# Performance work log

Measured on AMD Instinct MI355X. Metric: run time of the kernel, lower is better.

## Reference

```python
import jax, jax.numpy as jnp
import numpy as np

D_MODEL = 1024
NHEAD = 16
DIM_HEAD = 64
SCALE = DIM_HEAD ** (-0.5)


def setup_inputs() -> dict:
    key = jax.random.key(0)
    ks = jax.random.split(key, 8)
    B, N = 2, 2048
    inner = NHEAD * DIM_HEAD
    s = 0.02
    return {
        "query": jax.random.normal(ks[0], (B, N, D_MODEL), jnp.float32),
        "key": jax.random.normal(ks[1], (B, N, D_MODEL), jnp.float32),
        "value": jax.random.normal(ks[2], (B, N, D_MODEL), jnp.float32),
        "Wq": jax.random.normal(ks[3], (D_MODEL, inner), jnp.float32) * s,
        "Wk": jax.random.normal(ks[4], (D_MODEL, inner), jnp.float32) * s,
        "Wv": jax.random.normal(ks[5], (D_MODEL, inner), jnp.float32) * s,
        "Wo": jax.random.normal(ks[6], (inner, D_MODEL), jnp.float32) * s,
        "bo": jnp.zeros((D_MODEL,), jnp.float32),
    }


def reference(query, key, value, Wq, Wk, Wv, Wo, bo):
    B, Nq, _ = query.shape
    Nk = key.shape[1]
    # projections (no bias), split heads: [B, N, h, d]
    q = (query @ Wq).reshape(B, Nq, NHEAD, DIM_HEAD)
    k = (key @ Wk).reshape(B, Nk, NHEAD, DIM_HEAD)
    v = (value @ Wv).reshape(B, Nk, NHEAD, DIM_HEAD)
    # scores [B, h, Nq, Nk]
    sim = jnp.einsum('bihd,bjhd->bhij', q, k) * SCALE
    attn = jax.nn.softmax(sim, axis=-1)  # dropout p=0.0 -> identity
    out = jnp.einsum('bhij,bjhd->bihd', attn, v).reshape(B, Nq, NHEAD * DIM_HEAD)
    return out @ Wo + bo
```

## Files before the change

kernel.cpp:

```cpp
#include <hip/hip_runtime.h>
#include <stdint.h>

typedef __attribute__((ext_vector_type(8))) short short8;
typedef __attribute__((ext_vector_type(8))) unsigned short ushort8;
typedef __attribute__((ext_vector_type(4))) unsigned short ushort4v;
typedef __attribute__((ext_vector_type(4))) float float4v;
typedef _Float16 half4v __attribute__((ext_vector_type(4)));

#define D_MODEL 1024
#define NHEAD 16
#define DIM_HEAD 64
#define BATCH 2
#define SEQ 2048
#define BH (BATCH*NHEAD)
#define MROWS (BATCH*SEQ)
#define MK ((size_t)MROWS * D_MODEL)

__device__ __forceinline__ unsigned short f2bf(float f) {
  union { float f; unsigned u; } v; v.f = f;
  unsigned r = v.u + 0x7fffu + ((v.u >> 16) & 1u);
  return (unsigned short)(r >> 16);
}
__device__ __forceinline__ unsigned short f2bf_fast(float f) {
  union { float f; unsigned u; } v; v.f = f;
  return (unsigned short)((v.u + 0x8000u) >> 16);
}
__device__ __forceinline__ unsigned pk2bf(float a, float b) {
  union { float f; unsigned u; } x, y; x.f = a; y.f = b;
  return __builtin_amdgcn_perm(y.u + 0x8000u, x.u + 0x8000u, 0x07060302u);
}

__device__ __forceinline__ void gld16(const unsigned short* g, unsigned short* l) {
  __builtin_amdgcn_global_load_lds(
      (const __attribute__((address_space(1))) unsigned int*)g,
      (__attribute__((address_space(3))) unsigned int*)l, 16, 0, 0);
}

__global__ __launch_bounds__(256) void wtrans_kernel(const float* __restrict__ Wq,
    const float* __restrict__ Wk, const float* __restrict__ Wv,
    const float* __restrict__ Wo, unsigned short* __restrict__ WT0) {
  __shared__ float tile[32][33];
  const int z = blockIdx.z;
  const float* W = (z == 0) ? Wq : (z == 1) ? Wk : (z == 2) ? Wv : Wo;
  const float scale = (z == 0) ? 0.125f : 1.0f;
  unsigned short* WT = WT0 + ((size_t)z << 20);
  int bn = blockIdx.x * 32;
  int bk = blockIdx.y * 32;
  int tx = threadIdx.x & 31, ty = threadIdx.x >> 5;
#pragma unroll
  for (int i = 0; i < 4; i++)
    tile[ty + i*8][tx] = W[(size_t)(bk + ty + i*8) * D_MODEL + bn + tx];
  __syncthreads();
#pragma unroll
  for (int i = 0; i < 4; i++)
    WT[(size_t)(bn + ty + i*8) * D_MODEL + bk + tx] = f2bf(tile[tx][ty + i*8] * scale);
}

__global__ __launch_bounds__(256) void cast_kernel(const float* __restrict__ q,
    const float* __restrict__ k, const float* __restrict__ v,
    unsigned short* __restrict__ out) {
  const float* src = (blockIdx.y == 0) ? q : (blockIdx.y == 1) ? k : v;
  unsigned short* dst = out + (size_t)blockIdx.y * MK;
  size_t idx = ((size_t)blockIdx.x * 256 + threadIdx.x) * 8;
  float4v a = *(const float4v*)(src + idx);
  float4v b = *(const float4v*)(src + idx + 4);
  ushort8 o;
  o[0] = f2bf(a[0]); o[1] = f2bf(a[1]); o[2] = f2bf(a[2]); o[3] = f2bf(a[3]);
  o[4] = f2bf(b[0]); o[5] = f2bf(b[1]); o[6] = f2bf(b[2]); o[7] = f2bf(b[3]);
  *(ushort8*)(dst + idx) = o;
}

__global__ __launch_bounds__(256) void vtrans_kernel(const unsigned short* __restrict__ Vh,
                                                     unsigned short* __restrict__ VT) {
  __shared__ unsigned short tile[64][72];
  const int bh = blockIdx.x;
  const int n0 = blockIdx.y * 64;
  const int t = threadIdx.x;
#pragma unroll
  for (int p = 0; p < 2; p++) {
    int g = p*256 + t; int row = g >> 3, c = g & 7;
    *(ushort8*)&tile[row][c*8] =
      *(const ushort8*)(Vh + ((size_t)(bh*SEQ + n0 + row))*DIM_HEAD + c*8);
  }
  __syncthreads();
  int d = t >> 2, kc = (t & 3) * 16;
  ushort8 o0, o1;
#pragma unroll
  for (int j = 0; j < 8; j++) { o0[j] = tile[kc + j][d]; o1[j] = tile[kc + 8 + j][d]; }
  unsigned short* dst = VT + (((size_t)(bh*(SEQ/64) + blockIdx.y))*DIM_HEAD + d)*64 + kc;
  *(ushort8*)dst = o0;
  *(ushort8*)(dst + 8) = o1;
}

__global__ __launch_bounds__(256, 3) void proj_kernel(const unsigned short* __restrict__ Xbf,
    const unsigned short* __restrict__ WT0, unsigned short* __restrict__ Y0) {
  __shared__ unsigned short Al[128*64];
  __shared__ unsigned short Bl[128*64];
  const int z = blockIdx.z;
  const unsigned short* A  = Xbf + (size_t)z * MK;
  const unsigned short* BT = WT0 + ((size_t)z << 20);
  unsigned short* Y = Y0 + (size_t)z * MK;
  const int m0 = blockIdx.x * 128, n0 = blockIdx.y * 128;
  const int t = threadIdx.x;
  const int lane = t & 63, w = t >> 6, quad = lane >> 4, lid = lane & 15;
  const int wm = w & 1, wn = w >> 1;
  const int r8 = lane >> 3, c8 = (lane & 7) * 8;

  float4v acc[4][4];
#pragma unroll
  for (int i = 0; i < 4; i++)
#pragma unroll
    for (int j = 0; j < 4; j++) acc[i][j] = (float4v)0.0f;

  for (int k0 = 0; k0 < D_MODEL; k0 += 64) {
#pragma unroll
    for (int p = 0; p < 4; p++) {
      int seg = w*4 + p;
      gld16(A  + (size_t)(m0 + seg*8 + r8) * D_MODEL + k0 + c8, &Al[seg*8*64]);
      gld16(BT + (size_t)(n0 + seg*8 + r8) * D_MODEL + k0 + c8, &Bl[seg*8*64]);
    }
    __syncthreads();
#pragma unroll
    for (int kst = 0; kst < 2; kst++) {
      short8 af[4], bfr[4];
#pragma unroll
      for (int i = 0; i < 4; i++)
        af[i] = *(const short8*)&Al[(wm*64 + i*16 + lid)*64 + kst*32 + quad*8];
#pragma unroll
      for (int j = 0; j < 4; j++)
        bfr[j] = *(const short8*)&Bl[(wn*64 + j*16 + lid)*64 + kst*32 + quad*8];
#pragma unroll
      for (int i = 0; i < 4; i++)
#pragma unroll
        for (int j = 0; j < 4; j++)
          acc[i][j] = __builtin_amdgcn_mfma_f32_16x16x32_bf16(af[i], bfr[j], acc[i][j], 0, 0, 0);
    }
    __syncthreads();
  }
#pragma unroll
  for (int i = 0; i < 4; i++)
#pragma unroll
    for (int j = 0; j < 4; j++)
#pragma unroll
      for (int r = 0; r < 4; r++) {
        int row = m0 + wm*64 + i*16 + quad*4 + r;
        int col = n0 + wn*64 + j*16 + lid;
        int b = row >> 11, n = row & (SEQ - 1);
        int h = col >> 6,  d = col & 63;
        Y[(((size_t)(b*NHEAD + h))*SEQ + n)*DIM_HEAD + d] = f2bf_fast(acc[i][j][r]);
      }
}

__global__ __launch_bounds__(256, 3) void outproj_kernel(const unsigned short* __restrict__ A,
    const unsigned short* __restrict__ WT, const float* __restrict__ bias,
    float* __restrict__ out) {
  __shared__ unsigned short Al[64*64];
  __shared__ unsigned short Bl[128*64];
  const int m0 = blockIdx.x * 64, n0 = blockIdx.y * 128;
  const int t = threadIdx.x;
  const int lane = t & 63, w = t >> 6, quad = lane >> 4, lid = lane & 15;
  const int wm = w & 1, wn = w >> 1;
  const int r8 = lane >> 3, c8 = (lane & 7) * 8;

  float4v acc[2][4];
#pragma unroll
  for (int i = 0; i < 2; i++)
#pragma unroll
    for (int j = 0; j < 4; j++) acc[i][j] = (float4v)0.0f;

  for (int k0 = 0; k0 < D_MODEL; k0 += 64) {
#pragma unroll
    for (int p = 0; p < 2; p++) {
      int seg = w*2 + p;
      gld16(A + (size_t)(m0 + seg*8 + r8) * D_MODEL + k0 + c8, &Al[seg*8*64]);
    }
#pragma unroll
    for (int p = 0; p < 4; p++) {
      int seg = w*4 + p;
      gld16(WT + (size_t)(n0 + seg*8 + r8) * D_MODEL + k0 + c8, &Bl[seg*8*64]);
    }
    __syncthreads();
#pragma unroll
    for (int kst = 0; kst < 2; kst++) {
      short8 af[2], bfr[4];
#pragma unroll
      for (int i = 0; i < 2; i++)
        af[i] = *(const short8*)&Al[(wm*32 + i*16 + lid)*64 + kst*32 + quad*8];
#pragma unroll
      for (int j = 0; j < 4; j++)
        bfr[j] = *(const short8*)&Bl[(wn*64 + j*16 + lid)*64 + kst*32 + quad*8];
#pragma unroll
      for (int i = 0; i < 2; i++)
#pragma unroll
        for (int j = 0; j < 4; j++)
          acc[i][j] = __builtin_amdgcn_mfma_f32_16x16x32_bf16(af[i], bfr[j], acc[i][j], 0, 0, 0);
    }
    __syncthreads();
  }
#pragma unroll
  for (int i = 0; i < 2; i++)
#pragma unroll
    for (int j = 0; j < 4; j++)
#pragma unroll
      for (int r = 0; r < 4; r++) {
        int row = m0 + wm*32 + i*16 + quad*4 + r;
        int col = n0 + wn*64 + j*16 + lid;
        out[(size_t)row * D_MODEL + col] = acc[i][j][r] + bias[col];
      }
}

#define PSTR 68

__global__ __launch_bounds__(256, 2) void flash_kernel(const unsigned short* __restrict__ Q,
    const unsigned short* __restrict__ K, const unsigned short* __restrict__ VT,
    _Float16* __restrict__ Op0, _Float16* __restrict__ Op1,
    float* __restrict__ lpart) {
  __shared__ unsigned short Pl[4][4][16*PSTR];

  const int flat = blockIdx.x;
  const int bh  = (flat & 7) * 4 + ((flat >> 3) & 3);
  const int qz  = flat >> 5;
  const int qb  = qz & 7, z = qz >> 3;
  const int t = threadIdx.x;
  const int lane = t & 63, w = t >> 6, quad = lane >> 4, lid = lane & 15;
  const int q0 = qb * 256 + w * 64;
  const int kbeg = z * (SEQ/2);
  _Float16* Op = z ? Op1 : Op0;
  float* lp = lpart + (size_t)z * BH * SEQ;

  short8 qf[4][2];
#pragma unroll
  for (int st = 0; st < 4; st++)
#pragma unroll
    for (int kst = 0; kst < 2; kst++)
      qf[st][kst] = *(const short8*)(Q +
        ((size_t)(bh*SEQ + q0 + st*16 + lid))*DIM_HEAD + kst*32 + quad*8);

  float4v o[4][4];
#pragma unroll
  for (int st = 0; st < 4; st++)
#pragma unroll
    for (int i = 0; i < 4; i++) o[st][i] = (float4v)0.0f;
  float ps[4] = {0.0f, 0.0f, 0.0f, 0.0f};

  for (int kb = kbeg; kb < kbeg + SEQ/2; kb += 64) {
    short8 kf[2][4], vf[2][4];
#pragma unroll
    for (int kst = 0; kst < 2; kst++)
#pragma unroll
      for (int mb = 0; mb < 4; mb++)
        kf[kst][mb] = *(const short8*)(K +
          ((size_t)(bh*SEQ + kb + mb*16 + lid))*DIM_HEAD + kst*32 + quad*8);
    const unsigned short* Vp = VT + ((size_t)(bh*(SEQ/64) + (kb >> 6)))*DIM_HEAD*64;
#pragma unroll
    for (int kst = 0; kst < 2; kst++)
#pragma unroll
      for (int i = 0; i < 4; i++)
        vf[kst][i] = *(const short8*)(Vp + (size_t)(i*16 + lid)*64 + kst*32 + quad*8);

#pragma unroll
    for (int st = 0; st < 4; st++) {
      float4v s[4];
#pragma unroll
      for (int mb = 0; mb < 4; mb++) s[mb] = (float4v)0.0f;
#pragma unroll
      for (int kst = 0; kst < 2; kst++)
#pragma unroll
        for (int mb = 0; mb < 4; mb++)
          s[mb] = __builtin_amdgcn_mfma_f32_16x16x32_bf16(kf[kst][mb], qf[st][kst], s[mb], 0, 0, 0);

      unsigned short* Ptw = &Pl[w][st][0];
#pragma unroll
      for (int mb = 0; mb < 4; mb++) {
        float e0 = __expf(s[mb][0]);
        float e1 = __expf(s[mb][1]);
        float e2 = __expf(s[mb][2]);
        float e3 = __expf(s[mb][3]);
        ps[st] += (e0 + e1) + (e2 + e3);
        uint2 pk; pk.x = pk2bf(e0, e1); pk.y = pk2bf(e2, e3);
        *(uint2*)&Ptw[lid*PSTR + mb*16 + quad*4] = pk;
      }
      short8 pf0 = *(const short8*)&Ptw[lid*PSTR + quad*8];
      short8 pf1 = *(const short8*)&Ptw[lid*PSTR + 32 + quad*8];
#pragma unroll
      for (int i = 0; i < 4; i++) {
        o[st][i] = __builtin_amdgcn_mfma_f32_16x16x32_bf16(vf[0][i], pf0, o[st][i], 0, 0, 0);
        o[st][i] = __builtin_amdgcn_mfma_f32_16x16x32_bf16(vf[1][i], pf1, o[st][i], 0, 0, 0);
      }
    }
  }

#pragma unroll
  for (int st = 0; st < 4; st++) {
    float v = ps[st];
    v += __shfl_xor(v, 16); v += __shfl_xor(v, 32);
    int q = q0 + st*16 + lid;
    if (quad == 0) lp[(size_t)bh*SEQ + q] = v;
#pragma unroll
    for (int i = 0; i < 4; i++) {
      half4v hv;
#pragma unroll
      for (int r = 0; r < 4; r++) hv[r] = (_Float16)o[st][i][r];
      *(half4v*)(Op + ((size_t)bh*SEQ + q)*64 + i*16 + quad*4) = hv;
    }
  }
}

__global__ __launch_bounds__(256) void norm_kernel(const _Float16* __restrict__ Op0,
    const _Float16* __restrict__ Op1, const float* __restrict__ lpart,
    unsigned short* __restrict__ Ob) {
  int g = blockIdx.x * 256 + threadIdx.x;
  int d4 = g & 15, h = (g >> 4) & 15, q = (g >> 8) & (SEQ - 1), b = g >> 19;
  int bh = b * NHEAD + h;
  size_t obase = ((size_t)bh * SEQ + q) * 64 + d4 * 4;
  half4v a = *(const half4v*)(Op0 + obase);
  half4v c = *(const half4v*)(Op1 + obase);
  float l = lpart[(size_t)bh*SEQ + q] + lpart[(size_t)BH*SEQ + (size_t)bh*SEQ + q];
  float inv = 1.0f / l;
  float f0 = ((float)a[0] + (float)c[0]) * inv;
  float f1 = ((float)a[1] + (float)c[1]) * inv;
  float f2 = ((float)a[2] + (float)c[2]) * inv;
  float f3 = ((float)a[3] + (float)c[3]) * inv;
  uint2 pk; pk.x = pk2bf(f0, f1); pk.y = pk2bf(f2, f3);
  *(uint2*)&Ob[(((size_t)(b*SEQ + q))*NHEAD + h)*64 + d4*4] = pk;
}

extern "C" void kernel_launch(void* const* d_in, const int* in_sizes, int n_in,
                              void* d_out, int out_size, void* d_ws, size_t ws_size,
                              hipStream_t stream) {
  const float* query = (const float*)d_in[0];
  const float* key_  = (const float*)d_in[1];
  const float* value = (const float*)d_in[2];
  const float* Wq = (const float*)d_in[3];
  const float* Wk = (const float*)d_in[4];
  const float* Wv = (const float*)d_in[5];
  const float* Wo = (const float*)d_in[6];
  const float* bo = (const float*)d_in[7];
  float* out = (float*)d_out;

  char* ws = (char*)d_ws;
  unsigned short* WT0 = (unsigned short*)(ws);
  unsigned short* Xbf = (unsigned short*)(ws + (8ll  << 20));
  unsigned short* VT  = (unsigned short*)(ws + (8ll  << 20));
  unsigned short* Ob  = (unsigned short*)(ws + (16ll << 20));
  _Float16*       Op0 = (_Float16*)     (ws + (24ll << 20));
  unsigned short* Qb  = (unsigned short*)(ws + (32ll << 20));
  unsigned short* Kb  = (unsigned short*)(ws + (40ll << 20));
  unsigned short* Vb  = (unsigned short*)(ws + (48ll << 20));
  _Float16*       Op1 = (_Float16*)     (ws + (56ll << 20));
  float*          lp  = (float*)        (ws + (64ll << 20));

  dim3 tb(256);
  dim3 tg(32, 32, 4);
  hipLaunchKernelGGL(wtrans_kernel, tg, tb, 0, stream, Wq, Wk, Wv, Wo, WT0);

  dim3 cg(MK / (256*8), 3);
  hipLaunchKernelGGL(cast_kernel, cg, tb, 0, stream, query, key_, value, Xbf);

  dim3 pg(MROWS/128, D_MODEL/128, 3);
  hipLaunchKernelGGL(proj_kernel, pg, tb, 0, stream, Xbf, WT0, Qb);

  dim3 vg(BH, SEQ/64);
  hipLaunchKernelGGL(vtrans_kernel, vg, tb, 0, stream, Vb, VT);

  dim3 fg(512);
  hipLaunchKernelGGL(flash_kernel, fg, tb, 0, stream, Qb, Kb, VT, Op0, Op1, lp);

  dim3 ng((MROWS * NHEAD * DIM_HEAD / 4) / 256);
  hipLaunchKernelGGL(norm_kernel, ng, tb, 0, stream, Op0, Op1, lp, Ob);

  dim3 og(MROWS/64, D_MODEL/128);
  hipLaunchKernelGGL(outproj_kernel, og, tb, 0, stream, Ob, WT0 + (3ll << 20), bo, out);
}
```

Baseline: 245.6 us.

## Split flash attention key range four ways and raise occupancy

```diff
diff --git a/kernel.cpp b/kernel.cpp
--- a/kernel.cpp
+++ b/kernel.cpp
@@ -15,6 +15,7 @@
 #define BH (BATCH*NHEAD)
 #define MROWS (BATCH*SEQ)
 #define MK ((size_t)MROWS * D_MODEL)
+#define NSPLIT 4
 
 __device__ __forceinline__ unsigned short f2bf(float f) {
   union { float f; unsigned u; } v; v.f = f;
@@ -211,11 +212,10 @@
 
 #define PSTR 68
 
-__global__ __launch_bounds__(256, 2) void flash_kernel(const unsigned short* __restrict__ Q,
+__global__ __launch_bounds__(256, 4) void flash_kernel(const unsigned short* __restrict__ Q,
     const unsigned short* __restrict__ K, const unsigned short* __restrict__ VT,
-    _Float16* __restrict__ Op0, _Float16* __restrict__ Op1,
-    float* __restrict__ lpart) {
-  __shared__ unsigned short Pl[4][4][16*PSTR];
+    _Float16* __restrict__ Op0, float* __restrict__ lpart) {
+  __shared__ unsigned short Pl[4][2][16*PSTR];
 
   const int flat = blockIdx.x;
   const int bh  = (flat & 7) * 4 + ((flat >> 3) & 3);
@@ -224,8 +224,8 @@
   const int t = threadIdx.x;
   const int lane = t & 63, w = t >> 6, quad = lane >> 4, lid = lane & 15;
   const int q0 = qb * 256 + w * 64;
-  const int kbeg = z * (SEQ/2);
-  _Float16* Op = z ? Op1 : Op0;
+  const int kbeg = z * (SEQ/NSPLIT);
+  _Float16* Op = Op0 + (size_t)z * BH * SEQ * DIM_HEAD;
   float* lp = lpart + (size_t)z * BH * SEQ;
 
   short8 qf[4][2];
@@ -243,7 +243,7 @@
     for (int i = 0; i < 4; i++) o[st][i] = (float4v)0.0f;
   float ps[4] = {0.0f, 0.0f, 0.0f, 0.0f};
 
-  for (int kb = kbeg; kb < kbeg + SEQ/2; kb += 64) {
+  for (int kb = kbeg; kb < kbeg + SEQ/NSPLIT; kb += 64) {
     short8 kf[2][4], vf[2][4];
 #pragma unroll
     for (int kst = 0; kst < 2; kst++)
@@ -269,7 +269,7 @@
         for (int mb = 0; mb < 4; mb++)
           s[mb] = __builtin_amdgcn_mfma_f32_16x16x32_bf16(kf[kst][mb], qf[st][kst], s[mb], 0, 0, 0);
 
-      unsigned short* Ptw = &Pl[w][st][0];
+      unsigned short* Ptw = &Pl[w][st & 1][0];
 #pragma unroll
       for (int mb = 0; mb < 4; mb++) {
         float e0 = __expf(s[mb][0]);
@@ -306,21 +306,22 @@
   }
 }
 
-__global__ __launch_bounds__(256) void norm_kernel(const _Float16* __restrict__ Op0,
-    const _Float16* __restrict__ Op1, const float* __restrict__ lpart,
-    unsigned short* __restrict__ Ob) {
+__global__ __launch_bounds__(256) void norm_kernel(const _Float16* __restrict__ Op,
+    const float* __restrict__ lpart, unsigned short* __restrict__ Ob) {
   int g = blockIdx.x * 256 + threadIdx.x;
   int d4 = g & 15, h = (g >> 4) & 15, q = (g >> 8) & (SEQ - 1), b = g >> 19;
   int bh = b * NHEAD + h;
   size_t obase = ((size_t)bh * SEQ + q) * 64 + d4 * 4;
-  half4v a = *(const half4v*)(Op0 + obase);
-  half4v c = *(const half4v*)(Op1 + obase);
-  float l = lpart[(size_t)bh*SEQ + q] + lpart[(size_t)BH*SEQ + (size_t)bh*SEQ + q];
+  const size_t zstride = (size_t)BH * SEQ * DIM_HEAD;
+  float f0 = 0.f, f1 = 0.f, f2 = 0.f, f3 = 0.f, l = 0.f;
+#pragma unroll
+  for (int z = 0; z < NSPLIT; z++) {
+    half4v a = *(const half4v*)(Op + (size_t)z * zstride + obase);
+    f0 += (float)a[0]; f1 += (float)a[1]; f2 += (float)a[2]; f3 += (float)a[3];
+    l += lpart[(size_t)z * BH * SEQ + (size_t)bh * SEQ + q];
+  }
   float inv = 1.0f / l;
-  float f0 = ((float)a[0] + (float)c[0]) * inv;
-  float f1 = ((float)a[1] + (float)c[1]) * inv;
-  float f2 = ((float)a[2] + (float)c[2]) * inv;
-  float f3 = ((float)a[3] + (float)c[3]) * inv;
+  f0 *= inv; f1 *= inv; f2 *= inv; f3 *= inv;
   uint2 pk; pk.x = pk2bf(f0, f1); pk.y = pk2bf(f2, f3);
   *(uint2*)&Ob[(((size_t)(b*SEQ + q))*NHEAD + h)*64 + d4*4] = pk;
 }
@@ -343,12 +344,11 @@
   unsigned short* Xbf = (unsigned short*)(ws + (8ll  << 20));
   unsigned short* VT  = (unsigned short*)(ws + (8ll  << 20));
   unsigned short* Ob  = (unsigned short*)(ws + (16ll << 20));
-  _Float16*       Op0 = (_Float16*)     (ws + (24ll << 20));
   unsigned short* Qb  = (unsigned short*)(ws + (32ll << 20));
   unsigned short* Kb  = (unsigned short*)(ws + (40ll << 20));
   unsigned short* Vb  = (unsigned short*)(ws + (48ll << 20));
-  _Float16*       Op1 = (_Float16*)     (ws + (56ll << 20));
-  float*          lp  = (float*)        (ws + (64ll << 20));
+  _Float16*       Op  = (_Float16*)     (ws + (56ll << 20));
+  float*          lp  = (float*)        (ws + (88ll << 20));
 
   dim3 tb(256);
   dim3 tg(32, 32, 4);
@@ -363,11 +363,11 @@
   dim3 vg(BH, SEQ/64);
   hipLaunchKernelGGL(vtrans_kernel, vg, tb, 0, stream, Vb, VT);
 
-  dim3 fg(512);
-  hipLaunchKernelGGL(flash_kernel, fg, tb, 0, stream, Qb, Kb, VT, Op0, Op1, lp);
+  dim3 fg(1024);
+  hipLaunchKernelGGL(flash_kernel, fg, tb, 0, stream, Qb, Kb, VT, Op, lp);
 
   dim3 ng((MROWS * NHEAD * DIM_HEAD / 4) / 256);
-  hipLaunchKernelGGL(norm_kernel, ng, tb, 0, stream, Op0, Op1, lp, Ob);
+  hipLaunchKernelGGL(norm_kernel, ng, tb, 0, stream, Op, lp, Ob);
 
   dim3 og(MROWS/64, D_MODEL/128);
   hipLaunchKernelGGL(outproj_kernel, og, tb, 0, stream, Ob, WT0 + (3ll << 20), bo, out);
```

Measured after the change: 498.3 us. 2.03x slower.
